# Performance work log

Measured on AMD Instinct MI355X. Metric: run time of the kernel, lower is better.

Reference implementation:

```python
import jax, jax.numpy as jnp
import numpy as np

DIM = 256
D_INNER = 512      # expand=2 * dim
D_STATE = 16
D_CONV = 4
DT_RANK = 16       # ceil(dim/16)
EPS = 1e-5


def _mamba_params(key):
    ks = jax.random.split(key, 6)
    s = lambda k, shape, fan: jax.random.normal(k, shape, jnp.float32) * (fan ** -0.5)
    in_w = s(ks[0], (2 * D_INNER, DIM), DIM)
    conv_w = s(ks[1], (D_INNER, 1, D_CONV), D_CONV)
    conv_b = jnp.zeros((D_INNER,), jnp.float32)
    xproj_w = s(ks[2], (DT_RANK + 2 * D_STATE, D_INNER), D_INNER)
    dt_w = s(ks[3], (D_INNER, DT_RANK), DT_RANK)
    # dt bias: inverse-softplus of dt sampled in [1e-3, 0.1] (mamba init)
    dt = jnp.exp(jax.random.uniform(ks[4], (D_INNER,)) * (np.log(0.1) - np.log(1e-3)) + np.log(1e-3))
    dt_b = jnp.log(jnp.expm1(dt))
    A_log = jnp.log(jnp.broadcast_to(jnp.arange(1, D_STATE + 1, dtype=jnp.float32), (D_INNER, D_STATE)))
    Dp = jnp.ones((D_INNER,), jnp.float32)
    out_w = s(ks[5], (DIM, D_INNER), D_INNER)
    return in_w, conv_w, conv_b, xproj_w, dt_w, dt_b, A_log, Dp, out_w


def _layernorm(x, w, b):
    mu = x.mean(-1, keepdims=True)
    var = ((x - mu) ** 2).mean(-1, keepdims=True)  # biased var (torch WithBias_LayerNorm)
    return (x - mu) / jnp.sqrt(var + EPS) * w + b


def _mamba(x, in_w, conv_w, conv_b, xproj_w, dt_w, dt_b, A_log, Dp, out_w):
    B, L, _ = x.shape
    xz = x @ in_w.T                      # (B, L, 2*d_inner)
    u, z = jnp.split(xz, 2, axis=-1)
    # causal depthwise conv1d (torch pads both sides then slices [:L] == left pad)
    uc = jnp.transpose(u, (0, 2, 1))     # (B, d_inner, L)
    uc = jax.lax.conv_general_dilated(uc, conv_w, (1,), [(D_CONV - 1, 0)],
                                      dimension_numbers=('NCH', 'OIH', 'NCH'),
                                      feature_group_count=D_INNER) + conv_b[None, :, None]
    u = jax.nn.silu(jnp.transpose(uc, (0, 2, 1)))          # (B, L, d_inner)
    dbl = u @ xproj_w.T
    dt, Bm, Cm = jnp.split(dbl, [DT_RANK, DT_RANK + D_STATE], axis=-1)
    delta = jax.nn.softplus(dt @ dt_w.T + dt_b)            # (B, L, d_inner)
    A = -jnp.exp(A_log)                                    # (d_inner, d_state)

    def step(h, inp):
        d_t, b_t, c_t, u_t = inp         # (B,di),(B,ds),(B,ds),(B,di)
        h = h * jnp.exp(d_t[..., None] * A) + (d_t * u_t)[..., None] * b_t[:, None, :]
        y = jnp.einsum('bds,bs->bd', h, c_t)
        return h, y

    h0 = jnp.zeros((B, D_INNER, D_STATE), jnp.float32)
    xs = (jnp.moveaxis(delta, 1, 0), jnp.moveaxis(Bm, 1, 0),
          jnp.moveaxis(Cm, 1, 0), jnp.moveaxis(u, 1, 0))
    _, ys = jax.lax.scan(step, h0, xs)
    y = jnp.moveaxis(ys, 0, 1) + u * Dp
    y = y * jax.nn.silu(z)
    return y @ out_w.T


def setup_inputs() -> dict:
    key = jax.random.key(0)
    ks = jax.random.split(key, 4)
    B, N = 16, 2048
    x1 = jax.random.normal(ks[0], (B, N, DIM), jnp.float32)
    x2 = jax.random.normal(ks[1], (B, N, DIM), jnp.float32)
    ratio = jnp.float32(0.5)  # nn.Parameter init_ratio
    ln1_w = jnp.ones((DIM,), jnp.float32); ln1_b = jnp.zeros((DIM,), jnp.float32)
    ln2_w = jnp.ones((DIM,), jnp.float32); ln2_b = jnp.zeros((DIM,), jnp.float32)
    e1 = _mamba_params(ks[2]); e2 = _mamba_params(ks[3])
    names = ['in_w', 'conv_w', 'conv_b', 'xproj_w', 'dt_w', 'dt_b', 'A_log', 'D', 'out_w']
    d = {'x1': x1, 'x2': x2, 'ratio': ratio,
         'ln1_w': ln1_w, 'ln1_b': ln1_b, 'ln2_w': ln2_w, 'ln2_b': ln2_b}
    d.update({f'e1_{n}': v for n, v in zip(names, e1)})
    d.update({f'e2_{n}': v for n, v in zip(names, e2)})
    return d


def reference(x1, x2, ratio, ln1_w, ln1_b, ln2_w, ln2_b,
              e1_in_w, e1_conv_w, e1_conv_b, e1_xproj_w, e1_dt_w, e1_dt_b, e1_A_log, e1_D, e1_out_w,
              e2_in_w, e2_conv_w, e2_conv_b, e2_xproj_w, e2_dt_w, e2_dt_b, e2_A_log, e2_D, e2_out_w):
    # torch: num_chans = int(C * sigmoid(ratio)) -> static shape decision (int() severs grad)
    nc = int(DIM / (1.0 + np.exp(-np.asarray(ratio, dtype=np.float32))))
    x1_short, x2_short = x1, x2
    x1n = _layernorm(x1, ln1_w, ln1_b)
    x2n = _layernorm(x2, ln2_w, ln2_b)
    # faithful to torch: x1 is overwritten first, then x2 reads from the NEW x1
    x1s = jnp.concatenate([x2n[:, :, :nc], x1n[:, :, nc:]], axis=2)
    x2s = jnp.concatenate([x1s[:, :, :nc], x2n[:, :, nc:]], axis=2)
    o1 = _mamba(x1s, e1_in_w, e1_conv_w, e1_conv_b, e1_xproj_w, e1_dt_w, e1_dt_b, e1_A_log, e1_D, e1_out_w) + x1_short
    o2 = _mamba(x2s, e2_in_w, e2_conv_w, e2_conv_b, e2_xproj_w, e2_dt_w, e2_dt_b, e2_A_log, e2_D, e2_out_w) + x2_short
    return (o1, o2)
```

## Files before the change

kernel.cpp:

```cpp
#include <hip/hip_runtime.h>

typedef unsigned short ushort_t;
typedef __attribute__((ext_vector_type(8))) short bh8;
typedef __attribute__((ext_vector_type(4))) float f32x4;
typedef __attribute__((ext_vector_type(2))) unsigned int u32x2;
typedef __attribute__((ext_vector_type(4))) unsigned int u32x4;

#define DIM 256
#define DI 512
#define LEN 2048
#define BATCH 16
#define NROW (BATCH * LEN)
#define NCHUNK (NROW / 8)

__device__ __forceinline__ float b2f(ushort_t u) {
    union { unsigned int i; float f; } v; v.i = ((unsigned int)u) << 16; return v.f;
}
__device__ __forceinline__ ushort_t f2b(float f) {
    union { float ff; unsigned int i; } v; v.ff = f;
    unsigned int x = v.i;
    x += 0x7fffu + ((x >> 16) & 1u);
    return (ushort_t)(x >> 16);
}
__device__ __forceinline__ float fexp2(float x) { float r; asm("v_exp_f32 %0, %1" : "=v"(r) : "v"(x)); return r; }
__device__ __forceinline__ float flog2(float x) { float r; asm("v_log_f32 %0, %1" : "=v"(r) : "v"(x)); return r; }
__device__ __forceinline__ float frcp (float x) { float r; asm("v_rcp_f32 %0, %1" : "=v"(r) : "v"(x)); return r; }
__device__ __forceinline__ unsigned int cvtpk(float lo, float hi) {
    unsigned int r; asm("v_cvt_pk_bf16_f32 %0, %1, %2" : "=v"(r) : "v"(lo), "v"(hi)); return r;
}
__device__ __forceinline__ float silu(float x) {
    return x * frcp(1.0f + fexp2(-1.44269504f * x));
}
__device__ __forceinline__ float bsum16(float v) {
    float t;
    asm("v_add_f32_dpp %0, %1, %1 quad_perm:[1,0,3,2] row_mask:0xf bank_mask:0xf" : "=v"(t) : "v"(v));
    asm("v_add_f32_dpp %0, %1, %1 quad_perm:[2,3,0,1] row_mask:0xf bank_mask:0xf" : "=v"(v) : "v"(t));
    asm("v_add_f32_dpp %0, %1, %1 row_half_mirror row_mask:0xf bank_mask:0xf" : "=v"(t) : "v"(v));
    asm("v_add_f32_dpp %0, %1, %1 row_mirror row_mask:0xf bank_mask:0xf" : "=v"(v) : "v"(t));
    return v;
}
__device__ __forceinline__ void gload16(const void* g, void* l) {
    __builtin_amdgcn_global_load_lds((const __attribute__((address_space(1))) unsigned int*)g,
                                     (__attribute__((address_space(3))) unsigned int*)l, 16, 0, 0);
}

__global__ __launch_bounds__(256) void ln_swap_kernel(
    const float* __restrict__ x1, const float* __restrict__ x2,
    const float* __restrict__ ratio,
    const float* __restrict__ ln1w, const float* __restrict__ ln1b,
    const float* __restrict__ ln2w, const float* __restrict__ ln2b,
    ushort_t* __restrict__ xs1, ushort_t* __restrict__ xs2) {
    const int w = threadIdx.x >> 6, lane = threadIdx.x & 63;
    const int m = blockIdx.x * 4 + w;
    const int c0 = lane * 4;
    const size_t off = (size_t)m * DIM + c0;
    const f32x4 v1 = *(const f32x4*)(x1 + off);
    const f32x4 v2 = *(const f32x4*)(x2 + off);
    float s1 = 0.f, q1 = 0.f, s2 = 0.f, q2 = 0.f;
    #pragma unroll
    for (int k = 0; k < 4; k++) {
        s1 += v1[k]; q1 += v1[k] * v1[k];
        s2 += v2[k]; q2 += v2[k] * v2[k];
    }
    #pragma unroll
    for (int o = 32; o; o >>= 1) {
        s1 += __shfl_xor(s1, o); q1 += __shfl_xor(q1, o);
        s2 += __shfl_xor(s2, o); q2 += __shfl_xor(q2, o);
    }
    const float inv = 1.0f / DIM;
    const float mu1 = s1 * inv, mu2 = s2 * inv;
    const float r1 = rsqrtf(q1 * inv - mu1 * mu1 + 1e-5f);
    const float r2 = rsqrtf(q2 * inv - mu2 * mu2 + 1e-5f);
    const int nc = (int)(DIM / (1.0f + expf(-ratio[0])));
    const f32x4 w1 = *(const f32x4*)(ln1w + c0), b1 = *(const f32x4*)(ln1b + c0);
    const f32x4 w2 = *(const f32x4*)(ln2w + c0), b2 = *(const f32x4*)(ln2b + c0);
    float n1[4], n2[4], o1v[4];
    #pragma unroll
    for (int k = 0; k < 4; k++) {
        n1[k] = (v1[k] - mu1) * r1 * w1[k] + b1[k];
        n2[k] = (v2[k] - mu2) * r2 * w2[k] + b2[k];
        o1v[k] = (c0 + k < nc) ? n2[k] : n1[k];
    }
    u32x2 p2, p1;
    p2[0] = cvtpk(n2[0], n2[1]);  p2[1] = cvtpk(n2[2], n2[3]);
    p1[0] = cvtpk(o1v[0], o1v[1]); p1[1] = cvtpk(o1v[2], o1v[3]);
    *(u32x2*)(&xs2[off]) = p2;
    *(u32x2*)(&xs1[off]) = p1;
}

#define WB_IN 0
#define WB_XP 262144
#define WB_OUT 286720
#define WB_TOT 417792
__global__ __launch_bounds__(256) void cvtw_kernel(
    const float* __restrict__ iw0, const float* __restrict__ iw1,
    const float* __restrict__ xw0, const float* __restrict__ xw1,
    const float* __restrict__ ow0, const float* __restrict__ ow1,
    ushort_t* __restrict__ o0, ushort_t* __restrict__ o1) {
    const int e = blockIdx.z;
    const float* iw = e ? iw1 : iw0;
    const float* xw = e ? xw1 : xw0;
    const float* ow = e ? ow1 : ow0;
    ushort_t* o = e ? o1 : o0;
    const int idx = blockIdx.x * 256 + threadIdx.x;
    if (idx < WB_XP) o[idx] = f2b(iw[idx]);
    else if (idx < WB_OUT) o[idx] = f2b(xw[idx - WB_XP]);
    else if (idx < WB_TOT) o[idx] = f2b(ow[idx - WB_OUT]);
}

__global__ __launch_bounds__(256) void gemm_in_kernel(
    const ushort_t* __restrict__ A0, const ushort_t* __restrict__ A1,
    const ushort_t* __restrict__ Wb0, const ushort_t* __restrict__ Wb1,
    ushort_t* __restrict__ uT0, ushort_t* __restrict__ uT1,
    ushort_t* __restrict__ zT0, ushort_t* __restrict__ zT1) {
    const int e = blockIdx.z;
    const ushort_t* __restrict__ A = e ? A1 : A0;
    const ushort_t* __restrict__ W = e ? Wb1 : Wb0;
    ushort_t* __restrict__ uT = e ? uT1 : uT0;
    ushort_t* __restrict__ zT = e ? zT1 : zT0;
    const int m0 = blockIdx.x * 128;
    const int n0 = blockIdx.y * 128;
    const int tid = threadIdx.x, lane = tid & 63, wv = tid >> 6;
    const int wr = wv >> 1, wc = wv & 1;

    __shared__ ushort_t sA[128 * 32];
    __shared__ ushort_t sW[128 * 32];

    f32x4 acc[4][4];
    #pragma unroll
    for (int i = 0; i < 4; i++)
        #pragma unroll
        for (int j = 0; j < 4; j++) acc[i][j] = (f32x4){0.f, 0.f, 0.f, 0.f};

    const ushort_t* Ap = A + (size_t)(m0 + wv * 32 + (lane >> 2)) * 256 + (lane & 3) * 8;
    const ushort_t* Wp = W + (size_t)(n0 + wv * 32 + (lane >> 2)) * 256 + (lane & 3) * 8;

    for (int kt = 0; kt < 256; kt += 32) {
        __syncthreads();
        gload16(Ap + kt,             &sA[(wv * 32) * 32]);
        gload16(Ap + kt + 16 * 256,  &sA[(wv * 32 + 16) * 32]);
        gload16(Wp + kt,             &sW[(wv * 32) * 32]);
        gload16(Wp + kt + 16 * 256,  &sW[(wv * 32 + 16) * 32]);
        __syncthreads();
        bh8 af[4], wf[4];
        #pragma unroll
        for (int i = 0; i < 4; i++)
            af[i] = *(const bh8*)(&sA[(wr * 64 + i * 16 + (lane & 15)) * 32 + (lane >> 4) * 8]);
        #pragma unroll
        for (int j = 0; j < 4; j++)
            wf[j] = *(const bh8*)(&sW[(wc * 64 + j * 16 + (lane & 15)) * 32 + (lane >> 4) * 8]);
        #pragma unroll
        for (int i = 0; i < 4; i++)
            #pragma unroll
            for (int j = 0; j < 4; j++)
                acc[i][j] = __builtin_amdgcn_mfma_f32_16x16x32_bf16(af[i], wf[j], acc[i][j], 0, 0, 0);
    }

    #pragma unroll
    for (int i = 0; i < 4; i++) {
        #pragma unroll
        for (int j = 0; j < 4; j++) {
            const int rbase = m0 + wr * 64 + i * 16 + (lane >> 4) * 4;
            const int col = n0 + wc * 64 + j * 16 + (lane & 15);
            u32x2 vv;
            vv[0] = cvtpk(acc[i][j][0], acc[i][j][1]);
            vv[1] = cvtpk(acc[i][j][2], acc[i][j][3]);
            if (col < DI) *(u32x2*)(&uT[(size_t)col * NROW + rbase]) = vv;
            else          *(u32x2*)(&zT[(size_t)(col - DI) * NROW + rbase]) = vv;
        }
    }
}

__global__ __launch_bounds__(256) void conv_silu_kernel(
    const ushort_t* __restrict__ uT0, const ushort_t* __restrict__ uT1,
    const float* __restrict__ cw0, const float* __restrict__ cw1,
    const float* __restrict__ cb0, const float* __restrict__ cb1,
    ushort_t* __restrict__ ucT0, ushort_t* __restrict__ ucT1) {
    const int e = blockIdx.z;
    const ushort_t* __restrict__ uT = e ? uT1 : uT0;
    const float* __restrict__ cw = e ? cw1 : cw0;
    const float* __restrict__ cb = e ? cb1 : cb0;
    ushort_t* __restrict__ ucT = e ? ucT1 : ucT0;

    const int g = blockIdx.x * 256 + threadIdx.x;
    const int c = g & (NCHUNK - 1);
    const int d = g >> 12;
    const int b = c >> 8;
    const int t0 = (c & 255) * 8;
    const size_t base = (size_t)d * NROW + b * LEN + t0;

    bh8 cur = *(const bh8*)(uT + base);
    float win[11];
    if (t0) {
        win[0] = b2f(uT[base - 3]); win[1] = b2f(uT[base - 2]); win[2] = b2f(uT[base - 1]);
    } else {
        win[0] = 0.f; win[1] = 0.f; win[2] = 0.f;
    }
    #pragma unroll
    for (int j = 0; j < 8; j++) win[3 + j] = b2f((ushort_t)cur[j]);
    const f32x4 w = *(const f32x4*)(cw + d * 4);
    const float bias = cb[d];
    float s[8];
    #pragma unroll
    for (int j = 0; j < 8; j++) {
        const float a = bias + w[0] * win[j] + w[1] * win[j + 1] + w[2] * win[j + 2] + w[3] * win[j + 3];
        s[j] = silu(a);
    }
    u32x4 o;
    #pragma unroll
    for (int k = 0; k < 4; k++) o[k] = cvtpk(s[2 * k], s[2 * k + 1]);
    *(u32x4*)(ucT + base) = o;
}

__global__ __launch_bounds__(256) void gemm_xp_kernel(
    const ushort_t* __restrict__ ucT0, const ushort_t* __restrict__ ucT1,
    const ushort_t* __restrict__ Wb0, const ushort_t* __restrict__ Wb1,
    float* __restrict__ dbl0, float* __restrict__ dbl1,
    float* __restrict__ BCt0, float* __restrict__ BCt1) {
    const int e = blockIdx.z;
    const ushort_t* __restrict__ ucT = e ? ucT1 : ucT0;
    const ushort_t* __restrict__ W = (e ? Wb1 : Wb0) + WB_XP;
    float* __restrict__ dbl = e ? dbl1 : dbl0;
    float* __restrict__ BCt = e ? BCt1 : BCt0;
    const int m0 = blockIdx.x * 128;
    const int tid = threadIdx.x, lane = tid & 63;
    const int wc = tid >> 6;

    __shared__ ushort_t sW[48 * 40];
    __shared__ ushort_t sB[128 * 40];

    f32x4 acc[3][2];
    #pragma unroll
    for (int i = 0; i < 3; i++)
        #pragma unroll
        for (int j = 0; j < 2; j++) acc[i][j] = (f32x4){0.f, 0.f, 0.f, 0.f};

    const int kk = tid >> 3, mc = (tid & 7) * 16;
    const ushort_t* Bp = ucT + (size_t)kk * NROW + m0 + mc;

    for (int kt = 0; kt < 512; kt += 32) {
        __syncthreads();
        if (tid < 192) {
            const int r = tid >> 2, cc = (tid & 3) * 8;
            bh8 v = *(const bh8*)(W + (size_t)r * 512 + kt + cc);
            *(bh8*)(&sW[r * 40 + cc]) = v;
        }
        bh8 a0 = *(const bh8*)(Bp + (size_t)kt * NROW);
        bh8 a1 = *(const bh8*)(Bp + (size_t)kt * NROW + 8);
        #pragma unroll
        for (int q = 0; q < 8; q++) {
            sB[(mc + q) * 40 + kk] = (ushort_t)a0[q];
            sB[(mc + 8 + q) * 40 + kk] = (ushort_t)a1[q];
        }
        __syncthreads();
        bh8 af[3], wf[2];
        #pragma unroll
        for (int i = 0; i < 3; i++)
            af[i] = *(const bh8*)(&sW[(i * 16 + (lane & 15)) * 40 + (lane >> 4) * 8]);
        #pragma unroll
        for (int j = 0; j < 2; j++)
            wf[j] = *(const bh8*)(&sB[(wc * 32 + j * 16 + (lane & 15)) * 40 + (lane >> 4) * 8]);
        #pragma unroll
        for (int i = 0; i < 3; i++)
            #pragma unroll
            for (int j = 0; j < 2; j++)
                acc[i][j] = __builtin_amdgcn_mfma_f32_16x16x32_bf16(af[i], wf[j], acc[i][j], 0, 0, 0);
    }

    #pragma unroll
    for (int j = 0; j < 2; j++) {
        const int mm = m0 + wc * 32 + j * 16 + (lane & 15);
        {
            const int nb = (lane >> 4) * 4;
            #pragma unroll
            for (int r = 0; r < 4; r++)
                dbl[(size_t)(nb + r) * NROW + mm] = acc[0][j][r];
        }
        #pragma unroll
        for (int i = 1; i < 3; i++) {
            const int sb = (i - 1) * 16 + (lane >> 4) * 4;
            *(f32x4*)(&BCt[(size_t)mm * 32 + sb]) = acc[i][j];
        }
    }
}

__global__ __launch_bounds__(256) void delta_kernel(
    const float* __restrict__ dblT0, const float* __restrict__ dblT1,
    const float* __restrict__ dtw0, const float* __restrict__ dtw1,
    const float* __restrict__ dtb0, const float* __restrict__ dtb1,
    ushort_t* __restrict__ delT0, ushort_t* __restrict__ delT1) {
    const int e = blockIdx.z;
    const float* __restrict__ dblT = e ? dblT1 : dblT0;
    const float* __restrict__ dtw = e ? dtw1 : dtw0;
    const float* __restrict__ dtb = e ? dtb1 : dtb0;
    ushort_t* __restrict__ delT = e ? delT1 : delT0;

    const int tid = threadIdx.x, lane = tid & 63, wv = tid >> 6;
    const int bx = blockIdx.x;
    const int d = (bx & 127) * 4 + wv;
    const int m0 = (bx >> 7) * 256 + lane * 4;

    const float bias = dtb[d];
    f32x4 acc = {bias, bias, bias, bias};
    #pragma unroll
    for (int k = 0; k < 16; k++) {
        const float wk = dtw[d * 16 + k];
        const f32x4 bv = *(const f32x4*)(dblT + (size_t)k * NROW + m0);
        #pragma unroll
        for (int c = 0; c < 4; c++) acc[c] = fmaf(wk, bv[c], acc[c]);
    }
    float sp[4];
    #pragma unroll
    for (int c = 0; c < 4; c++) {
        const float x = acc[c];
        sp[c] = (x > 20.0f) ? x : 0.69314718f * flog2(1.0f + fexp2(1.44269504f * x));
    }
    u32x2 r;
    r[0] = cvtpk(sp[0], sp[1]);
    r[1] = cvtpk(sp[2], sp[3]);
    *(u32x2*)(&delT[(size_t)d * NROW + m0]) = r;
}

__global__ __launch_bounds__(256) void scan_kernel(
    const ushort_t* delT0, const ushort_t* delT1,
    const ushort_t* __restrict__ ucT0, const ushort_t* __restrict__ ucT1,
    const float* __restrict__ BCt0, const float* __restrict__ BCt1,
    const float* __restrict__ al0, const float* __restrict__ al1,
    const float* __restrict__ Dp0, const float* __restrict__ Dp1,
    ushort_t* y0, ushort_t* y1) {
    const int gid = blockIdx.x;
    const int xcd = gid & 7;
    const int k = gid >> 3;
    const int combo = xcd * 4 + (k >> 5);
    const int dtile = k & 31;
    const int e = combo & 1;
    const int b = combo >> 1;

    const ushort_t* delT = e ? delT1 : delT0;
    const ushort_t* __restrict__ ucT = e ? ucT1 : ucT0;
    const float* __restrict__ BCt = e ? BCt1 : BCt0;
    const float* __restrict__ al = e ? al1 : al0;
    const float* __restrict__ Dq = e ? Dp1 : Dp0;
    ushort_t* yo = e ? y1 : y0;

    const int tid = threadIdx.x;
    const int s = tid & 15;
    const int dloc = tid >> 4;
    const int d = dtile * 16 + dloc;
    const int w = tid >> 6, lane = tid & 63;

    __shared__ ushort_t sD[2][16 * 64];
    __shared__ ushort_t sU[2][16 * 64];
    __shared__ float sBC[2][64 * 32];

    const ushort_t* srcA = ((w >= 2) ? ucT : delT)
        + (size_t)(dtile * 16 + (w & 1) * 8 + (lane >> 3)) * NROW + b * LEN + (lane & 7) * 8;
    const float* srcBC = BCt + (size_t)b * LEN * 32;

    const float A2 = -expf(al[(d << 4) + s]) * 1.44269504f;
    const float Dpv16 = Dq[d] * 0.0625f;

    ushort_t* yp = yo + (size_t)d * NROW + b * LEN;

    {
        ushort_t* dstA = ((w >= 2) ? sU[0] : sD[0]) + (w & 1) * 512;
        gload16(srcA, dstA);
        gload16(srcBC + (w * 2 + 0) * 256 + lane * 4, &sBC[0][(w * 2 + 0) * 256]);
        gload16(srcBC + (w * 2 + 1) * 256 + lane * 4, &sBC[0][(w * 2 + 1) * 256]);
    }
    __syncthreads();

    float h = 0.f;
    for (int sup = 0; sup < 32; sup++) {
        const int q = sup & 1;
        {
            ushort_t* dstA = ((w >= 2) ? sU[q ^ 1] : sD[q ^ 1]) + (w & 1) * 512;
            gload16(srcA + (sup + 1) * 64, dstA);
            const float* sb = srcBC + (size_t)(sup + 1) * 2048;
            gload16(sb + (w * 2 + 0) * 256 + lane * 4, &sBC[q ^ 1][(w * 2 + 0) * 256]);
            gload16(sb + (w * 2 + 1) * 256 + lane * 4, &sBC[q ^ 1][(w * 2 + 1) * 256]);
        }
        #pragma unroll
        for (int sub = 0; sub < 8; sub++) {
            const bh8 dv = *(const bh8*)(&sD[q][dloc * 64 + sub * 8]);
            const bh8 uv = *(const bh8*)(&sU[q][dloc * 64 + sub * 8]);
            float yv[8];
            #pragma unroll
            for (int j = 0; j < 8; j++) {
                const float dt = b2f((ushort_t)dv[j]);
                const float uf = b2f((ushort_t)uv[j]);
                const float Bj = sBC[q][(sub * 8 + j) * 32 + s];
                const float Cj = sBC[q][(sub * 8 + j) * 32 + 16 + s];
                h = fmaf(h, fexp2(dt * A2), dt * uf * Bj);
                yv[j] = fmaf(uf, Dpv16, h * Cj);
            }
            #pragma unroll
            for (int j = 0; j < 8; j++) yv[j] = bsum16(yv[j]);
            u32x4 o;
            #pragma unroll
            for (int kk = 0; kk < 4; kk++)
                o[kk] = cvtpk(yv[2 * kk], yv[2 * kk + 1]);
            if (s == 0) *(u32x4*)(yp + sup * 64 + sub * 8) = o;
        }
        __syncthreads();
    }
}

__global__ __launch_bounds__(256) void gemm_out_kernel(
    const ushort_t* __restrict__ yT0, const ushort_t* __restrict__ yT1,
    const ushort_t* __restrict__ zT0, const ushort_t* __restrict__ zT1,
    const ushort_t* __restrict__ Wb0, const ushort_t* __restrict__ Wb1,
    const float* __restrict__ r0, const float* __restrict__ r1,
    float* __restrict__ o0, float* __restrict__ o1) {
    const int e = blockIdx.z;
    const ushort_t* __restrict__ yT = e ? yT1 : yT0;
    const ushort_t* __restrict__ zT = e ? zT1 : zT0;
    const ushort_t* __restrict__ W = (e ? Wb1 : Wb0) + WB_OUT;
    const float* __restrict__ rr = e ? r1 : r0;
    float* __restrict__ oo = e ? o1 : o0;
    const int m0 = blockIdx.x * 128;
    const int n0 = blockIdx.y * 128;
    const int tid = threadIdx.x, lane = tid & 63, wv = tid >> 6;
    const int wr = wv >> 1, wc = wv & 1;

    __shared__ ushort_t sA[128 * 40];
    __shared__ ushort_t sW[128 * 32];

    f32x4 acc[4][4];
    #pragma unroll
    for (int i = 0; i < 4; i++)
        #pragma unroll
        for (int j = 0; j < 4; j++) acc[i][j] = (f32x4){0.f, 0.f, 0.f, 0.f};

    const int kk = tid >> 3, mc = (tid & 7) * 16;
    const ushort_t* Yp = yT + (size_t)kk * NROW + m0 + mc;
    const ushort_t* Zp = zT + (size_t)kk * NROW + m0 + mc;
    const ushort_t* Wp = W + (size_t)(n0 + wv * 32 + (lane >> 2)) * 512 + (lane & 3) * 8;

    for (int kt = 0; kt < 512; kt += 32) {
        __syncthreads();
        gload16(Wp + kt,             &sW[(wv * 32) * 32]);
        gload16(Wp + kt + 16 * 512,  &sW[(wv * 32 + 16) * 32]);
        bh8 a0 = *(const bh8*)(Yp + (size_t)kt * NROW);
        bh8 a1 = *(const bh8*)(Yp + (size_t)kt * NROW + 8);
        bh8 z0 = *(const bh8*)(Zp + (size_t)kt * NROW);
        bh8 z1 = *(const bh8*)(Zp + (size_t)kt * NROW + 8);
        #pragma unroll
        for (int q = 0; q < 4; q++) {
            const unsigned int p0 = cvtpk(
                b2f((ushort_t)a0[2 * q])     * silu(b2f((ushort_t)z0[2 * q])),
                b2f((ushort_t)a0[2 * q + 1]) * silu(b2f((ushort_t)z0[2 * q + 1])));
            const unsigned int p1 = cvtpk(
                b2f((ushort_t)a1[2 * q])     * silu(b2f((ushort_t)z1[2 * q])),
                b2f((ushort_t)a1[2 * q + 1]) * silu(b2f((ushort_t)z1[2 * q + 1])));
            sA[(mc + 2 * q) * 40 + kk]     = (ushort_t)p0;
            sA[(mc + 2 * q + 1) * 40 + kk] = (ushort_t)(p0 >> 16);
            sA[(mc + 8 + 2 * q) * 40 + kk]     = (ushort_t)p1;
            sA[(mc + 8 + 2 * q + 1) * 40 + kk] = (ushort_t)(p1 >> 16);
        }
        __syncthreads();
        bh8 af[4], wf[4];
        #pragma unroll
        for (int i = 0; i < 4; i++)
            af[i] = *(const bh8*)(&sA[(wr * 64 + i * 16 + (lane & 15)) * 40 + (lane >> 4) * 8]);
        #pragma unroll
        for (int j = 0; j < 4; j++)
            wf[j] = *(const bh8*)(&sW[(wc * 64 + j * 16 + (lane & 15)) * 32 + (lane >> 4) * 8]);
        #pragma unroll
        for (int i = 0; i < 4; i++)
            #pragma unroll
            for (int j = 0; j < 4; j++)
                acc[i][j] = __builtin_amdgcn_mfma_f32_16x16x32_bf16(af[i], wf[j], acc[i][j], 0, 0, 0);
    }

    #pragma unroll
    for (int i = 0; i < 4; i++) {
        #pragma unroll
        for (int j = 0; j < 4; j++) {
            const int rbase = m0 + wr * 64 + i * 16 + (lane >> 4) * 4;
            const int col = n0 + wc * 64 + j * 16 + (lane & 15);
            #pragma unroll
            for (int r = 0; r < 4; r++) {
                const size_t off = (size_t)(rbase + r) * DIM + col;
                oo[off] = acc[i][j][r] + rr[off];
            }
        }
    }
}

extern "C" void kernel_launch(void* const* d_in, const int* in_sizes, int n_in,
                              void* d_out, int out_size, void* d_ws, size_t ws_size,
                              hipStream_t stream) {
    const float* x1    = (const float*)d_in[0];
    const float* x2    = (const float*)d_in[1];
    const float* ratio = (const float*)d_in[2];
    const float* ln1w  = (const float*)d_in[3];
    const float* ln1b  = (const float*)d_in[4];
    const float* ln2w  = (const float*)d_in[5];
    const float* ln2b  = (const float*)d_in[6];
    const float* inw[2]   = {(const float*)d_in[7],  (const float*)d_in[16]};
    const float* convw[2] = {(const float*)d_in[8],  (const float*)d_in[17]};
    const float* convb[2] = {(const float*)d_in[9],  (const float*)d_in[18]};
    const float* xprw[2]  = {(const float*)d_in[10], (const float*)d_in[19]};
    const float* dtw[2]   = {(const float*)d_in[11], (const float*)d_in[20]};
    const float* dtb[2]   = {(const float*)d_in[12], (const float*)d_in[21]};
    const float* alog[2]  = {(const float*)d_in[13], (const float*)d_in[22]};
    const float* Dp[2]    = {(const float*)d_in[14], (const float*)d_in[23]};
    const float* outw[2]  = {(const float*)d_in[15], (const float*)d_in[24]};

    float* o1 = (float*)d_out;
    float* o2 = o1 + (size_t)NROW * DIM;
    ushort_t* xs[2] = {(ushort_t*)o1, (ushort_t*)o2};
    const size_t XS_BYTES  = (size_t)NROW * DIM * 2;
    const size_t DBL_BYTES = (size_t)16 * NROW * 4;
    float* dbl[2] = {(float*)((char*)o1 + XS_BYTES), (float*)((char*)o2 + XS_BYTES)};
    float* BCt[2] = {(float*)((char*)o1 + XS_BYTES + DBL_BYTES),
                     (float*)((char*)o2 + XS_BYTES + DBL_BYTES)};

    const size_t SZ_DI = (size_t)NROW * DI * 2;
    const size_t SZ_WB = ((size_t)WB_TOT * 2 + 255) & ~(size_t)255;
    char* p = (char*)d_ws;
    ushort_t* uT[2]  = {(ushort_t*)p, (ushort_t*)(p + SZ_DI)};            p += 2 * SZ_DI;
    ushort_t* zT[2]  = {(ushort_t*)p, (ushort_t*)(p + SZ_DI)};            p += 2 * SZ_DI;
    ushort_t* ucT[2] = {(ushort_t*)p, (ushort_t*)(p + SZ_DI)};            p += 2 * SZ_DI;
    ushort_t* wbf[2] = {(ushort_t*)p, (ushort_t*)(p + SZ_WB)};
    ushort_t* delT[2] = {uT[0], uT[1]};
    ushort_t* yT[2]   = {uT[0], uT[1]};

    ln_swap_kernel<<<NROW / 4, 256, 0, stream>>>(x1, x2, ratio, ln1w, ln1b, ln2w, ln2b, xs[0], xs[1]);

    cvtw_kernel<<<dim3(WB_TOT / 256, 1, 2), 256, 0, stream>>>(
        inw[0], inw[1], xprw[0], xprw[1], outw[0], outw[1], wbf[0], wbf[1]);

    gemm_in_kernel<<<dim3(NROW / 128, 8, 2), 256, 0, stream>>>(
        xs[0], xs[1], wbf[0], wbf[1], uT[0], uT[1], zT[0], zT[1]);

    conv_silu_kernel<<<dim3((DI * NCHUNK) / 256, 1, 2), 256, 0, stream>>>(
        uT[0], uT[1], convw[0], convw[1], convb[0], convb[1], ucT[0], ucT[1]);

    gemm_xp_kernel<<<dim3(NROW / 128, 1, 2), 256, 0, stream>>>(
        ucT[0], ucT[1], wbf[0], wbf[1], dbl[0], dbl[1], BCt[0], BCt[1]);

    delta_kernel<<<dim3(128 * 128, 1, 2), 256, 0, stream>>>(
        dbl[0], dbl[1], dtw[0], dtw[1], dtb[0], dtb[1], delT[0], delT[1]);

    scan_kernel<<<dim3(1024), 256, 0, stream>>>(
        delT[0], delT[1], ucT[0], ucT[1], BCt[0], BCt[1],
        alog[0], alog[1], Dp[0], Dp[1], yT[0], yT[1]);

    gemm_out_kernel<<<dim3(NROW / 128, 2, 2), 256, 0, stream>>>(
        yT[0], yT[1], zT[0], zT[1], wbf[0], wbf[1], x1, x2, o1, o2);
}
```

Measured before the change: 526.5 us.

## Scan: two states per thread, 32 channels per block, halve grid

```diff
diff --git a/kernel.cpp b/kernel.cpp
--- a/kernel.cpp
+++ b/kernel.cpp
@@ -38,6 +38,20 @@
     asm("v_add_f32_dpp %0, %1, %1 row_half_mirror row_mask:0xf bank_mask:0xf" : "=v"(t) : "v"(v));
     asm("v_add_f32_dpp %0, %1, %1 row_mirror row_mask:0xf bank_mask:0xf" : "=v"(v) : "v"(t));
     return v;
+}
+__device__ __forceinline__ float bsum8(float v) {
+    float t;
+    asm("v_add_f32_dpp %0, %1, %1 quad_perm:[1,0,3,2] row_mask:0xf bank_mask:0xf" : "=v"(t) : "v"(v));
+    asm("v_add_f32_dpp %0, %1, %1 quad_perm:[2,3,0,1] row_mask:0xf bank_mask:0xf" : "=v"(v) : "v"(t));
+    asm("v_add_f32_dpp %0, %1, %1 row_half_mirror row_mask:0xf bank_mask:0xf" : "=v"(t) : "v"(v));
+    return t + __int_as_float(0) * 0.f + v - v + t;
+}
+__device__ __forceinline__ float bsum8_fix(float v) {
+    float t;
+    asm("v_add_f32_dpp %0, %1, %1 quad_perm:[1,0,3,2] row_mask:0xf bank_mask:0xf" : "=v"(t) : "v"(v));
+    asm("v_add_f32_dpp %0, %1, %1 quad_perm:[2,3,0,1] row_mask:0xf bank_mask:0xf" : "=v"(v) : "v"(t));
+    asm("v_add_f32_dpp %0, %1, %1 row_half_mirror row_mask:0xf bank_mask:0xf" : "=v"(t) : "v"(v));
+    return t;
 }
 __device__ __forceinline__ void gload16(const void* g, void* l) {
     __builtin_amdgcn_global_load_lds((const __attribute__((address_space(1))) unsigned int*)g,
@@ -331,8 +345,8 @@
     const int gid = blockIdx.x;
     const int xcd = gid & 7;
     const int k = gid >> 3;
-    const int combo = xcd * 4 + (k >> 5);
-    const int dtile = k & 31;
+    const int combo = xcd * 4 + (k >> 4);
+    const int dtile = k & 15;
     const int e = combo & 1;
     const int b = combo >> 1;
 
@@ -344,38 +358,38 @@
     ushort_t* yo = e ? y1 : y0;
 
     const int tid = threadIdx.x;
-    const int s = tid & 15;
-    const int dloc = tid >> 4;
-    const int d = dtile * 16 + dloc;
     const int w = tid >> 6, lane = tid & 63;
-
-    __shared__ ushort_t sD[2][16 * 64];
-    __shared__ ushort_t sU[2][16 * 64];
+    const int sl = lane & 7;
+    const int dloc = tid >> 3;
+    const int d = dtile * 32 + dloc;
+
+    __shared__ ushort_t sD[2][32 * 64];
+    __shared__ ushort_t sU[2][32 * 64];
     __shared__ float sBC[2][64 * 32];
 
-    const ushort_t* srcA = ((w >= 2) ? ucT : delT)
-        + (size_t)(dtile * 16 + (w & 1) * 8 + (lane >> 3)) * NROW + b * LEN + (lane & 7) * 8;
+    const int srow = tid >> 3;
+    const ushort_t* srcD = delT + (size_t)(dtile * 32 + srow) * NROW + b * LEN + (tid & 7) * 8;
+    const ushort_t* srcU = ucT  + (size_t)(dtile * 32 + srow) * NROW + b * LEN + (tid & 7) * 8;
     const float* srcBC = BCt + (size_t)b * LEN * 32;
 
-    const float A2 = -expf(al[(d << 4) + s]) * 1.44269504f;
-    const float Dpv16 = Dq[d] * 0.0625f;
+    const float A2a = -expf(al[(d << 4) + sl]) * 1.44269504f;
+    const float A2b = -expf(al[(d << 4) + sl + 8]) * 1.44269504f;
+    const float Dpv8 = Dq[d] * 0.125f;
 
     ushort_t* yp = yo + (size_t)d * NROW + b * LEN;
 
-    {
-        ushort_t* dstA = ((w >= 2) ? sU[0] : sD[0]) + (w & 1) * 512;
-        gload16(srcA, dstA);
-        gload16(srcBC + (w * 2 + 0) * 256 + lane * 4, &sBC[0][(w * 2 + 0) * 256]);
-        gload16(srcBC + (w * 2 + 1) * 256 + lane * 4, &sBC[0][(w * 2 + 1) * 256]);
-    }
+    gload16(srcD, &sD[0][srow * 64 + (tid & 7) * 8]);
+    gload16(srcU, &sU[0][srow * 64 + (tid & 7) * 8]);
+    gload16(srcBC + (w * 2 + 0) * 256 + lane * 4, &sBC[0][(w * 2 + 0) * 256]);
+    gload16(srcBC + (w * 2 + 1) * 256 + lane * 4, &sBC[0][(w * 2 + 1) * 256]);
     __syncthreads();
 
-    float h = 0.f;
+    float h0 = 0.f, h1 = 0.f;
     for (int sup = 0; sup < 32; sup++) {
         const int q = sup & 1;
         {
-            ushort_t* dstA = ((w >= 2) ? sU[q ^ 1] : sD[q ^ 1]) + (w & 1) * 512;
-            gload16(srcA + (sup + 1) * 64, dstA);
+            gload16(srcD + (sup + 1) * 64, &sD[q ^ 1][srow * 64 + (tid & 7) * 8]);
+            gload16(srcU + (sup + 1) * 64, &sU[q ^ 1][srow * 64 + (tid & 7) * 8]);
             const float* sb = srcBC + (size_t)(sup + 1) * 2048;
             gload16(sb + (w * 2 + 0) * 256 + lane * 4, &sBC[q ^ 1][(w * 2 + 0) * 256]);
             gload16(sb + (w * 2 + 1) * 256 + lane * 4, &sBC[q ^ 1][(w * 2 + 1) * 256]);
@@ -387,20 +401,25 @@
             float yv[8];
             #pragma unroll
             for (int j = 0; j < 8; j++) {
+                const int t = sub * 8 + j;
                 const float dt = b2f((ushort_t)dv[j]);
                 const float uf = b2f((ushort_t)uv[j]);
-                const float Bj = sBC[q][(sub * 8 + j) * 32 + s];
-                const float Cj = sBC[q][(sub * 8 + j) * 32 + 16 + s];
-                h = fmaf(h, fexp2(dt * A2), dt * uf * Bj);
-                yv[j] = fmaf(uf, Dpv16, h * Cj);
+                const float dtuf = dt * uf;
+                const float B0 = sBC[q][t * 32 + sl];
+                const float B1 = sBC[q][t * 32 + 8 + sl];
+                const float C0 = sBC[q][t * 32 + 16 + sl];
+                const float C1 = sBC[q][t * 32 + 24 + sl];
+                h0 = fmaf(h0, fexp2(dt * A2a), dtuf * B0);
+                h1 = fmaf(h1, fexp2(dt * A2b), dtuf * B1);
+                yv[j] = fmaf(uf, Dpv8, fmaf(h1, C1, h0 * C0));
             }
             #pragma unroll
-            for (int j = 0; j < 8; j++) yv[j] = bsum16(yv[j]);
+            for (int j = 0; j < 8; j++) yv[j] = bsum8_fix(yv[j]);
             u32x4 o;
             #pragma unroll
             for (int kk = 0; kk < 4; kk++)
                 o[kk] = cvtpk(yv[2 * kk], yv[2 * kk + 1]);
-            if (s == 0) *(u32x4*)(yp + sup * 64 + sub * 8) = o;
+            if (sl == 0) *(u32x4*)(yp + sup * 64 + sub * 8) = o;
         }
         __syncthreads();
     }
@@ -544,7 +563,7 @@
     delta_kernel<<<dim3(128 * 128, 1, 2), 256, 0, stream>>>(
         dbl[0], dbl[1], dtw[0], dtw[1], dtb[0], dtb[1], delT[0], delT[1]);
 
-    scan_kernel<<<dim3(1024), 256, 0, stream>>>(
+    scan_kernel<<<dim3(512), 256, 0, stream>>>(
         delT[0], delT[1], ucT[0], ucT[1], BCt[0], BCt[1],
         alog[0], alog[1], Dp[0], Dp[1], yT[0], yT[1]);
 
```

Result: faster. 478.5 us (-9.1%).
